# Kernel tuning notes

Measured on AMD Instinct MI355X. Metric: run time of the kernel, lower is better.

## Reference

```python
import jax, jax.numpy as jnp
import numpy as np

N_USER = 50000
N_ITEM = 100000
EMB = 64
NNZ = 1200000
BATCH = 4096
RATE = 0.1          # node_dropout[0]
N_LAYERS = 4        # len(layer_size); make_hop needs >=4 hops for 5 prefix means
N_NODES = N_USER + N_ITEM


def setup_inputs() -> dict:
    key = jax.random.key(0)
    ks = jax.random.split(key, 12)
    return {
        "user_emb": jax.random.normal(ks[0], (N_USER, EMB), dtype=jnp.float32) * 0.1,
        "item_emb": jax.random.normal(ks[1], (N_ITEM, EMB), dtype=jnp.float32) * 0.1,
        "adj_vals": jax.random.uniform(ks[2], (NNZ,), dtype=jnp.float32),
        "drop_u": jax.random.uniform(ks[3], (NNZ,), dtype=jnp.float32),
        "adj_rows": jax.random.randint(ks[4], (NNZ,), 0, N_NODES, dtype=jnp.int32),
        "adj_cols": jax.random.randint(ks[5], (NNZ,), 0, N_NODES, dtype=jnp.int32),
        "users": jax.random.randint(ks[6], (BATCH,), 0, N_USER, dtype=jnp.int32),
        "pos_items": jax.random.randint(ks[7], (BATCH,), 0, N_ITEM, dtype=jnp.int32),
        "neg_items": jax.random.randint(ks[8], (BATCH,), 0, N_ITEM, dtype=jnp.int32),
        "u_a": jax.random.randint(ks[9], (BATCH,), 0, 5, dtype=jnp.int32),
        "p_a": jax.random.randint(ks[10], (BATCH,), 0, 5, dtype=jnp.int32),
        "n_a": jax.random.randint(ks[11], (BATCH,), 0, 5, dtype=jnp.int32),
        "index": 0,
    }


def _make_hop(user_emb, item_emb, adj_vals, drop_u, adj_rows, adj_cols):
    # sparse dropout: floor(1 - rate + u) gives a 0/1 keep mask; rescale by 1/(1-rate).
    mask = jnp.floor((1.0 - RATE) + drop_u)
    vals = adj_vals * mask * (1.0 / (1.0 - RATE))
    ego = jnp.concatenate([user_emb, item_emb], axis=0)  # [N, d]
    all_embs = [ego]
    for _ in range(N_LAYERS):
        # SpMM: out[r] = sum_e vals[e] * ego[cols[e]] for rows[e] == r
        msgs = vals[:, None] * ego[adj_cols]             # [nnz, d]
        ego = jax.ops.segment_sum(msgs, adj_rows, num_segments=N_NODES)
        all_embs.append(ego)
    # prefix means over hops 0..i
    result = [all_embs[0]]
    running = all_embs[0]
    for i in range(1, 5):
        running = running + all_embs[i]
        result.append(running / float(i + 1))
    return jnp.stack(result)  # [5, N, d]


def reference(user_emb, item_emb, adj_vals, drop_u, adj_rows, adj_cols,
              users, pos_items, neg_items, u_a, p_a, n_a, index):
    embed = _make_hop(user_emb, item_emb, adj_vals, drop_u, adj_rows, adj_cols)
    n_user = user_emb.shape[0]
    if index == 0:
        u = embed[u_a, users]
        p = embed[p_a, pos_items + n_user]
        n = embed[n_a, neg_items + n_user]
    else:
        u = embed[u_a, users + n_user]
        p = embed[p_a, pos_items]
        n = embed[n_a, neg_items]
    return (u, p, n)
```

## Files before the change

### kernel.cpp

```cpp
#include <hip/hip_runtime.h>
#include <stdint.h>

#define N_USER_C  50000
#define N_ITEM_C  100000
#define N_NODES_C 150000
#define EMB_C     64
#define NNZ_C     1200000
#define BATCH_C   4096

#define BKT_SHIFT 9
#define BKT_ROWS  (1 << BKT_SHIFT)
#define NB        ((N_NODES_C + BKT_ROWS - 1) / BKT_ROWS)
#define CH        8192
#define NBLK      ((NNZ_C + CH - 1) / CH)
#define N2        (NB * NBLK)
#define COL_MASK  0x3FFFF

#define SPMM_B    37500
#define GB        3072
#define THB       2048

typedef _Float16 h16;
typedef _Float16 h16x4 __attribute__((ext_vector_type(4)));

__global__ __launch_bounds__(1024) void k_bin_count(const float* __restrict__ du,
                                                    const int* __restrict__ rows,
                                                    int* __restrict__ cnt2,
                                                    int* __restrict__ flagz) {
    __shared__ int bk[NB];
    int t = threadIdx.x, blk = blockIdx.x;
    for (int i = blk * 1024 + t; i < 2 * N_NODES_C; i += NBLK * 1024) flagz[i] = 0;
    for (int i = t; i < NB; i += 1024) bk[i] = 0;
    __syncthreads();
    int base = blk * CH;
    for (int i = 0; i < CH; i += 1024) {
        int e = base + i + t;
        if (e < NNZ_C && floorf(0.9f + du[e]) != 0.0f)
            atomicAdd(&bk[rows[e] >> BKT_SHIFT], 1);
    }
    __syncthreads();
    for (int i = t; i < NB; i += 1024) cnt2[i * NBLK + blk] = bk[i];
}

__global__ __launch_bounds__(512) void k_bbase(const int* __restrict__ cnt2,
                                               int* __restrict__ bbase,
                                               int* __restrict__ base2,
                                               int* __restrict__ row_start) {
    __shared__ int sh[512];
    int t = threadIdx.x;
    int s = 0;
    if (t < NB) {
        const int* p = cnt2 + t * NBLK;
        for (int i = 0; i < NBLK; ++i) s += p[i];
    }
    sh[t] = s;
    __syncthreads();
    for (int off = 1; off < 512; off <<= 1) {
        int v = (t >= off) ? sh[t - off] : 0;
        __syncthreads();
        sh[t] += v;
        __syncthreads();
    }
    if (t < NB) bbase[t] = sh[t] - s;
    if (t == 511) {
        base2[N2] = sh[511];
        row_start[N_NODES_C] = sh[511];
    }
}

__global__ __launch_bounds__(256) void k_bscan(const int* __restrict__ cnt2,
                                               const int* __restrict__ bbase,
                                               int* __restrict__ base2) {
    __shared__ int sh[256];
    int t = threadIdx.x, i = blockIdx.x;
    int v0 = (t < NBLK) ? cnt2[i * NBLK + t] : 0;
    sh[t] = v0;
    __syncthreads();
    for (int off = 1; off < 256; off <<= 1) {
        int v = (t >= off) ? sh[t - off] : 0;
        __syncthreads();
        sh[t] += v;
        __syncthreads();
    }
    if (t < NBLK) base2[i * NBLK + t] = bbase[i] + sh[t] - v0;
}

__global__ __launch_bounds__(1024) void k_bin_write(const float* __restrict__ av,
                                                    const float* __restrict__ du,
                                                    const int* __restrict__ rows,
                                                    const int* __restrict__ cols,
                                                    const int* __restrict__ base2,
                                                    int2* __restrict__ ev) {
    __shared__ int cur[NB];
    int t = threadIdx.x, blk = blockIdx.x;
    for (int i = t; i < NB; i += 1024) cur[i] = base2[i * NBLK + blk];
    __syncthreads();
    int base = blk * CH;
    for (int i = 0; i < CH; i += 1024) {
        int e = base + i + t;
        if (e < NNZ_C) {
            float m = floorf(0.9f + du[e]);
            if (m != 0.0f) {
                float v = av[e] * m * (float)(1.0 / 0.9);
                int r = rows[e];
                int pos = atomicAdd(&cur[r >> BKT_SHIFT], 1);
                int2 p;
                p.x = ((r & (BKT_ROWS - 1)) << 18) | cols[e];
                p.y = __float_as_int(v);
                ev[pos] = p;
            }
        }
    }
}

__global__ __launch_bounds__(256) void k_bucket_sort(const int2* __restrict__ ev,
                                                     const int* __restrict__ base2,
                                                     int2* __restrict__ ep,
                                                     int* __restrict__ row_start) {
    __shared__ int rowcnt[BKT_ROWS];
    __shared__ int cursor[BKT_ROWS];
    __shared__ int tsum[256];
    int t = threadIdx.x, k = blockIdx.x;
    int rowBase = k << BKT_SHIFT;
    int bstart = base2[k * NBLK];
    int bend   = base2[(k + 1) * NBLK];
    for (int i = t; i < BKT_ROWS; i += 256) rowcnt[i] = 0;
    __syncthreads();
    for (int e = bstart + t; e < bend; e += 256)
        atomicAdd(&rowcnt[((unsigned)ev[e].x) >> 18], 1);
    __syncthreads();
    int a = rowcnt[2 * t], b = rowcnt[2 * t + 1];
    tsum[t] = a + b;
    __syncthreads();
    for (int off = 1; off < 256; off <<= 1) {
        int v = (t >= off) ? tsum[t - off] : 0;
        __syncthreads();
        tsum[t] += v;
        __syncthreads();
    }
    int excl = tsum[t] - (a + b);
    cursor[2 * t]     = excl;
    cursor[2 * t + 1] = excl + a;
    int gr = rowBase + 2 * t;
    if (gr < N_NODES_C)     row_start[gr]     = bstart + excl;
    if (gr + 1 < N_NODES_C) row_start[gr + 1] = bstart + excl + a;
    __syncthreads();
    for (int e = bstart + t; e < bend; e += 256) {
        int2 p = ev[e];
        int rl = ((unsigned)p.x) >> 18;
        int slot = atomicAdd(&cursor[rl], 1);
        p.x &= COL_MASK;
        ep[bstart + slot] = p;
    }
}

__device__ __forceinline__ void batch_row_a(int wid, int idx0,
                                            const int* __restrict__ users,
                                            const int* __restrict__ pos,
                                            const int* __restrict__ neg,
                                            const int* __restrict__ ua,
                                            const int* __restrict__ pa,
                                            const int* __restrict__ na,
                                            int& row, int& a) {
    int s = wid >> 12;
    int j = wid & (BATCH_C - 1);
    if (s == 0)      { row = users[j] + (idx0 ? N_USER_C : 0); a = ua[j]; }
    else if (s == 1) { row = pos[j]   + (idx0 ? 0 : N_USER_C); a = pa[j]; }
    else             { row = neg[j]   + (idx0 ? 0 : N_USER_C); a = na[j]; }
}

__device__ __forceinline__ void spmm_row_body(int wid, int lane,
                                              const int* __restrict__ rs,
                                              const int2* __restrict__ ep,
                                              const h16x4* __restrict__ ego,
                                              h16x4* __restrict__ nxt,
                                              const int* __restrict__ flag) {
    if (wid >= N_NODES_C) return;
    if (flag && flag[wid] == 0) return;
    int start = rs[wid];
    int end   = rs[wid + 1];
    int eo = lane >> 4;
    int l  = lane & 15;
    float4 acc = make_float4(0.f, 0.f, 0.f, 0.f);
    #pragma unroll 2
    for (int it = start + eo; it < end; it += 4) {
        int2 p = ep[it];
        float v = __int_as_float(p.y);
        h16x4 g = ego[(int64_t)p.x * 16 + l];
        acc.x += v * (float)g[0]; acc.y += v * (float)g[1];
        acc.z += v * (float)g[2]; acc.w += v * (float)g[3];
    }
    acc.x += __shfl_xor(acc.x, 16); acc.y += __shfl_xor(acc.y, 16);
    acc.z += __shfl_xor(acc.z, 16); acc.w += __shfl_xor(acc.w, 16);
    acc.x += __shfl_xor(acc.x, 32); acc.y += __shfl_xor(acc.y, 32);
    acc.z += __shfl_xor(acc.z, 32); acc.w += __shfl_xor(acc.w, 32);
    if (lane < 16) {
        h16x4 h;
        h[0] = (h16)acc.x; h[1] = (h16)acc.y; h[2] = (h16)acc.z; h[3] = (h16)acc.w;
        nxt[(int64_t)wid * 16 + l] = h;
    }
}

__device__ __forceinline__ void gather_body(const h16* __restrict__ src,
                                            float* __restrict__ out, int t, int hop,
                                            int idx0,
                                            const int* __restrict__ users,
                                            const int* __restrict__ pos,
                                            const int* __restrict__ neg,
                                            const int* __restrict__ ua,
                                            const int* __restrict__ pa,
                                            const int* __restrict__ na) {
    int d = t & 63;
    int b = t >> 6;
    int row, a;
    batch_row_a(b, idx0, users, pos, neg, ua, pa, na, row, a);
    if (hop <= a)
        out[t] += (float)src[(int64_t)row * EMB_C + d] / (float)(a + 1);
}

__global__ __launch_bounds__(256) void k_prep(const float* __restrict__ ue,
                                              const float* __restrict__ ie,
                                              h16x4* __restrict__ dst,
                                              float* __restrict__ out,
                                              const int* __restrict__ users,
                                              const int* __restrict__ pos,
                                              const int* __restrict__ neg,
                                              const int* __restrict__ ua,
                                              const int* __restrict__ pa,
                                              const int* __restrict__ na,
                                              const int* __restrict__ indexp) {
    if (blockIdx.x < GB) {
        int t = blockIdx.x * 256 + threadIdx.x;
        int d = t & 63;
        int b = t >> 6;
        int row, a;
        batch_row_a(b, indexp[0], users, pos, neg, ua, pa, na, row, a);
        const float* sp = (row < N_USER_C) ? (ue + (int64_t)row * EMB_C)
                                           : (ie + (int64_t)(row - N_USER_C) * EMB_C);
        out[t] = sp[d] / (float)(a + 1);
    } else {
        const int totalU = N_USER_C * EMB_C / 4;
        const int total  = N_NODES_C * EMB_C / 4;
        const int stride = THB * 256;
        const float4* uev = (const float4*)ue;
        const float4* iev = (const float4*)ie;
        for (int i = (blockIdx.x - GB) * 256 + threadIdx.x; i < total; i += stride) {
            float4 v = (i < totalU) ? uev[i] : iev[i - totalU];
            h16x4 h;
            h[0] = (h16)v.x; h[1] = (h16)v.y; h[2] = (h16)v.z; h[3] = (h16)v.w;
            dst[i] = h;
        }
    }
}

__global__ __launch_bounds__(256) void k_spmm1f(const int* __restrict__ rs,
                                                const int2* __restrict__ ep,
                                                const h16x4* __restrict__ ego,
                                                h16x4* __restrict__ nxt,
                                                int* __restrict__ flag3,
                                                int* __restrict__ flag2,
                                                const int* __restrict__ users,
                                                const int* __restrict__ pos,
                                                const int* __restrict__ neg,
                                                const int* __restrict__ ua,
                                                const int* __restrict__ pa,
                                                const int* __restrict__ na,
                                                const int* __restrict__ indexp) {
    int lane = threadIdx.x & 63;
    if (blockIdx.x < SPMM_B) {
        int wid = (blockIdx.x * 256 + threadIdx.x) >> 6;
        spmm_row_body(wid, lane, rs, ep, ego, nxt, (const int*)nullptr);
    } else {
        int wid = ((blockIdx.x - SPMM_B) * 256 + threadIdx.x) >> 6;
        if (wid >= 3 * BATCH_C) return;
        int row, a;
        batch_row_a(wid, indexp[0], users, pos, neg, ua, pa, na, row, a);
        if (a < 2) return;
        if (lane == 0) {
            flag2[row] = 1;
            if (a >= 3) flag3[row] = 1;
        }
        if (a == 4) {
            int start = rs[row], end = rs[row + 1];
            for (int e = start + lane; e < end; e += 64)
                flag3[ep[e].x] = 1;
        }
    }
}

__global__ __launch_bounds__(256) void k_fg1(const int* __restrict__ rs,
                                             const int2* __restrict__ ep,
                                             const int* __restrict__ flag3,
                                             int* __restrict__ flag2,
                                             const h16* __restrict__ src,
                                             float* __restrict__ out,
                                             const int* __restrict__ users,
                                             const int* __restrict__ pos,
                                             const int* __restrict__ neg,
                                             const int* __restrict__ ua,
                                             const int* __restrict__ pa,
                                             const int* __restrict__ na,
                                             const int* __restrict__ indexp) {
    if (blockIdx.x < SPMM_B) {
        int wid  = (blockIdx.x * 256 + threadIdx.x) >> 6;
        int lane = threadIdx.x & 63;
        if (wid >= N_NODES_C || flag3[wid] == 0) return;
        int start = rs[wid], end = rs[wid + 1];
        for (int e = start + lane; e < end; e += 64)
            flag2[ep[e].x] = 1;
    } else {
        int t = (blockIdx.x - SPMM_B) * 256 + threadIdx.x;
        gather_body(src, out, t, 1, indexp[0], users, pos, neg, ua, pa, na);
    }
}

__global__ __launch_bounds__(256) void k_spmm2(const int* __restrict__ rs,
                                               const int2* __restrict__ ep,
                                               const h16x4* __restrict__ ego,
                                               h16x4* __restrict__ nxt,
                                               const int* __restrict__ flag) {
    int wid  = (blockIdx.x * 256 + threadIdx.x) >> 6;
    int lane = threadIdx.x & 63;
    spmm_row_body(wid, lane, rs, ep, ego, nxt, flag);
}

__global__ __launch_bounds__(256) void k_spmm3g2(const int* __restrict__ rs,
                                                 const int2* __restrict__ ep,
                                                 const h16x4* __restrict__ ego,
                                                 h16x4* __restrict__ nxt,
                                                 const int* __restrict__ flag3,
                                                 const h16* __restrict__ gsrc,
                                                 float* __restrict__ out,
                                                 const int* __restrict__ users,
                                                 const int* __restrict__ pos,
                                                 const int* __restrict__ neg,
                                                 const int* __restrict__ ua,
                                                 const int* __restrict__ pa,
                                                 const int* __restrict__ na,
                                                 const int* __restrict__ indexp) {
    if (blockIdx.x < SPMM_B) {
        int wid  = (blockIdx.x * 256 + threadIdx.x) >> 6;
        int lane = threadIdx.x & 63;
        spmm_row_body(wid, lane, rs, ep, ego, nxt, flag3);
    } else {
        int t = (blockIdx.x - SPMM_B) * 256 + threadIdx.x;
        gather_body(gsrc, out, t, 2, indexp[0], users, pos, neg, ua, pa, na);
    }
}

__global__ __launch_bounds__(256) void k_g3g4(const int* __restrict__ rs,
                                              const int2* __restrict__ ep,
                                              const h16x4* __restrict__ ego,
                                              float* __restrict__ out,
                                              const int* __restrict__ users,
                                              const int* __restrict__ pos,
                                              const int* __restrict__ neg,
                                              const int* __restrict__ ua,
                                              const int* __restrict__ pa,
                                              const int* __restrict__ na,
                                              const int* __restrict__ indexp) {
    int gid  = blockIdx.x * 256 + threadIdx.x;
    int wid  = gid >> 6;
    int lane = gid & 63;
    if (wid >= 3 * BATCH_C) return;
    int row, a;
    batch_row_a(wid, indexp[0], users, pos, neg, ua, pa, na, row, a);
    if (a < 3) return;
    float4 acc = make_float4(0.f, 0.f, 0.f, 0.f);
    if (a == 4) {
        int start = rs[row], end = rs[row + 1];
        int eo = lane >> 4;
        int l  = lane & 15;
        for (int it = start + eo; it < end; it += 4) {
            int2 p = ep[it];
            float v = __int_as_float(p.y);
            h16x4 g = ego[(int64_t)p.x * 16 + l];
            acc.x += v * (float)g[0]; acc.y += v * (float)g[1];
            acc.z += v * (float)g[2]; acc.w += v * (float)g[3];
        }
        acc.x += __shfl_xor(acc.x, 16); acc.y += __shfl_xor(acc.y, 16);
        acc.z += __shfl_xor(acc.z, 16); acc.w += __shfl_xor(acc.w, 16);
        acc.x += __shfl_xor(acc.x, 32); acc.y += __shfl_xor(acc.y, 32);
        acc.z += __shfl_xor(acc.z, 32); acc.w += __shfl_xor(acc.w, 32);
    }
    if (lane < 16) {
        h16x4 g = ego[(int64_t)row * 16 + lane];
        float inv = 1.0f / (float)(a + 1);
        float4* o = (float4*)out + (int64_t)wid * 16 + lane;
        float4 cv = *o;
        cv.x += ((float)g[0] + acc.x) * inv;
        cv.y += ((float)g[1] + acc.y) * inv;
        cv.z += ((float)g[2] + acc.z) * inv;
        cv.w += ((float)g[3] + acc.w) * inv;
        *o = cv;
    }
}

extern "C" void kernel_launch(void* const* d_in, const int* in_sizes, int n_in,
                              void* d_out, int out_size, void* d_ws, size_t ws_size,
                              hipStream_t stream) {
    const float* user_emb = (const float*)d_in[0];
    const float* item_emb = (const float*)d_in[1];
    const float* adj_vals = (const float*)d_in[2];
    const float* drop_u   = (const float*)d_in[3];
    const int*   adj_rows = (const int*)d_in[4];
    const int*   adj_cols = (const int*)d_in[5];
    const int*   users    = (const int*)d_in[6];
    const int*   pos_it   = (const int*)d_in[7];
    const int*   neg_it   = (const int*)d_in[8];
    const int*   u_a      = (const int*)d_in[9];
    const int*   p_a      = (const int*)d_in[10];
    const int*   n_a      = (const int*)d_in[11];
    const int*   indexp   = (const int*)d_in[12];
    float* out = (float*)d_out;

    const size_t egoElems = (size_t)N_NODES_C * EMB_C;
    h16*   egoH0     = (h16*)d_ws;
    h16*   bufA      = egoH0 + egoElems;
    h16*   bufB      = bufA + egoElems;
    int2*  ep        = (int2*)(bufB + egoElems);
    int2*  ev        = ep + NNZ_C;
    int*   row_start = (int*)(ev + NNZ_C);
    int*   cnt2      = row_start + N_NODES_C + 1;
    int*   base2     = cnt2 + N2 + 1;
    int*   bbase     = base2 + N2 + 1;
    int*   flags3    = bbase + NB + 1;
    int*   flags2    = flags3 + N_NODES_C;

    k_bin_count<<<NBLK, 1024, 0, stream>>>(drop_u, adj_rows, cnt2, flags3);
    k_bbase<<<1, 512, 0, stream>>>(cnt2, bbase, base2, row_start);
    k_bscan<<<NB, 256, 0, stream>>>(cnt2, bbase, base2);
    k_bin_write<<<NBLK, 1024, 0, stream>>>(adj_vals, drop_u, adj_rows, adj_cols,
                                           base2, ev);
    k_bucket_sort<<<NB, 256, 0, stream>>>(ev, base2, ep, row_start);

    k_prep<<<GB + THB, 256, 0, stream>>>(user_emb, item_emb, (h16x4*)egoH0, out,
                                         users, pos_it, neg_it, u_a, p_a, n_a, indexp);

    k_spmm1f<<<SPMM_B + GB, 256, 0, stream>>>(row_start, ep, (const h16x4*)egoH0,
                                              (h16x4*)bufA, flags3, flags2,
                                              users, pos_it, neg_it, u_a, p_a, n_a, indexp);
    k_fg1<<<SPMM_B + GB, 256, 0, stream>>>(row_start, ep, flags3, flags2,
                                           bufA, out,
                                           users, pos_it, neg_it, u_a, p_a, n_a, indexp);
    k_spmm2<<<SPMM_B, 256, 0, stream>>>(row_start, ep, (const h16x4*)bufA,
                                        (h16x4*)bufB, flags2);
    k_spmm3g2<<<SPMM_B + GB, 256, 0, stream>>>(row_start, ep, (const h16x4*)bufB,
                                               (h16x4*)bufA, flags3, bufB, out,
                                               users, pos_it, neg_it, u_a, p_a, n_a, indexp);
    k_g3g4<<<GB, 256, 0, stream>>>(row_start, ep, (const h16x4*)bufA, out,
                                   users, pos_it, neg_it, u_a, p_a, n_a, indexp);
}
```

Baseline: 194.1 us.

## Merge bucket-base scans into one kernel and move flag marking into prep

Replaces the single-block bucket-total scan plus per-bucket scan with one kernel in which each block recomputes its prefix by reducing all earlier counts. Separately, the batch-row flag-marking work moves from the first SpMM launch into the prep kernel as extra blocks, leaving a pure SpMM kernel. This removes a launch and a serial single-block step, at the cost of redundant reads of the count array (quadratic in bucket count) across blocks.

Measured after the change: 205.5 us. 1.06x slower.

```diff
diff --git a/kernel.cpp b/kernel.cpp
--- a/kernel.cpp
+++ b/kernel.cpp
@@ -19,6 +19,7 @@
 #define SPMM_B    37500
 #define GB        3072
 #define THB       2048
+#define FB        3072
 
 typedef _Float16 h16;
 typedef _Float16 h16x4 __attribute__((ext_vector_type(4)));
@@ -42,38 +43,23 @@
     for (int i = t; i < NB; i += 1024) cnt2[i * NBLK + blk] = bk[i];
 }
 
-__global__ __launch_bounds__(512) void k_bbase(const int* __restrict__ cnt2,
-                                               int* __restrict__ bbase,
-                                               int* __restrict__ base2,
-                                               int* __restrict__ row_start) {
-    __shared__ int sh[512];
-    int t = threadIdx.x;
-    int s = 0;
-    if (t < NB) {
-        const int* p = cnt2 + t * NBLK;
-        for (int i = 0; i < NBLK; ++i) s += p[i];
-    }
-    sh[t] = s;
-    __syncthreads();
-    for (int off = 1; off < 512; off <<= 1) {
-        int v = (t >= off) ? sh[t - off] : 0;
-        __syncthreads();
-        sh[t] += v;
-        __syncthreads();
-    }
-    if (t < NB) bbase[t] = sh[t] - s;
-    if (t == 511) {
-        base2[N2] = sh[511];
-        row_start[N_NODES_C] = sh[511];
-    }
-}
-
-__global__ __launch_bounds__(256) void k_bscan(const int* __restrict__ cnt2,
-                                               const int* __restrict__ bbase,
-                                               int* __restrict__ base2) {
+__global__ __launch_bounds__(256) void k_bscan2(const int* __restrict__ cnt2,
+                                                int* __restrict__ base2,
+                                                int* __restrict__ row_start) {
+    __shared__ int red[256];
     __shared__ int sh[256];
     int t = threadIdx.x, i = blockIdx.x;
-    int v0 = (t < NBLK) ? cnt2[i * NBLK + t] : 0;
+    int lim = i * NBLK;
+    int s = 0;
+    for (int idx = t; idx < lim; idx += 256) s += cnt2[idx];
+    red[t] = s;
+    __syncthreads();
+    for (int off = 128; off > 0; off >>= 1) {
+        if (t < off) red[t] += red[t + off];
+        __syncthreads();
+    }
+    int pre = red[0];
+    int v0 = (t < NBLK) ? cnt2[lim + t] : 0;
     sh[t] = v0;
     __syncthreads();
     for (int off = 1; off < 256; off <<= 1) {
@@ -82,7 +68,12 @@
         sh[t] += v;
         __syncthreads();
     }
-    if (t < NBLK) base2[i * NBLK + t] = bbase[i] + sh[t] - v0;
+    if (t < NBLK) base2[lim + t] = pre + sh[t] - v0;
+    if (i == NB - 1 && t == NBLK - 1) {
+        int total = pre + sh[t];
+        base2[N2] = total;
+        row_start[N_NODES_C] = total;
+    }
 }
 
 __global__ __launch_bounds__(1024) void k_bin_write(const float* __restrict__ av,
@@ -222,6 +213,10 @@
                                               const float* __restrict__ ie,
                                               h16x4* __restrict__ dst,
                                               float* __restrict__ out,
+                                              const int* __restrict__ rs,
+                                              const int2* __restrict__ ep,
+                                              int* __restrict__ flag3,
+                                              int* __restrict__ flag2,
                                               const int* __restrict__ users,
                                               const int* __restrict__ pos,
                                               const int* __restrict__ neg,
@@ -238,7 +233,7 @@
         const float* sp = (row < N_USER_C) ? (ue + (int64_t)row * EMB_C)
                                            : (ie + (int64_t)(row - N_USER_C) * EMB_C);
         out[t] = sp[d] / (float)(a + 1);
-    } else {
+    } else if (blockIdx.x < GB + THB) {
         const int totalU = N_USER_C * EMB_C / 4;
         const int total  = N_NODES_C * EMB_C / 4;
         const int stride = THB * 256;
@@ -250,28 +245,9 @@
             h[0] = (h16)v.x; h[1] = (h16)v.y; h[2] = (h16)v.z; h[3] = (h16)v.w;
             dst[i] = h;
         }
-    }
-}
-
-__global__ __launch_bounds__(256) void k_spmm1f(const int* __restrict__ rs,
-                                                const int2* __restrict__ ep,
-                                                const h16x4* __restrict__ ego,
-                                                h16x4* __restrict__ nxt,
-                                                int* __restrict__ flag3,
-                                                int* __restrict__ flag2,
-                                                const int* __restrict__ users,
-                                                const int* __restrict__ pos,
-                                                const int* __restrict__ neg,
-                                                const int* __restrict__ ua,
-                                                const int* __restrict__ pa,
-                                                const int* __restrict__ na,
-                                                const int* __restrict__ indexp) {
-    int lane = threadIdx.x & 63;
-    if (blockIdx.x < SPMM_B) {
-        int wid = (blockIdx.x * 256 + threadIdx.x) >> 6;
-        spmm_row_body(wid, lane, rs, ep, ego, nxt, (const int*)nullptr);
     } else {
-        int wid = ((blockIdx.x - SPMM_B) * 256 + threadIdx.x) >> 6;
+        int wid  = ((blockIdx.x - GB - THB) * 256 + threadIdx.x) >> 6;
+        int lane = threadIdx.x & 63;
         if (wid >= 3 * BATCH_C) return;
         int row, a;
         batch_row_a(wid, indexp[0], users, pos, neg, ua, pa, na, row, a);
@@ -286,6 +262,15 @@
                 flag3[ep[e].x] = 1;
         }
     }
+}
+
+__global__ __launch_bounds__(256) void k_spmm1(const int* __restrict__ rs,
+                                               const int2* __restrict__ ep,
+                                               const h16x4* __restrict__ ego,
+                                               h16x4* __restrict__ nxt) {
+    int wid  = (blockIdx.x * 256 + threadIdx.x) >> 6;
+    int lane = threadIdx.x & 63;
+    spmm_row_body(wid, lane, rs, ep, ego, nxt, (const int*)nullptr);
 }
 
 __global__ __launch_bounds__(256) void k_fg1(const int* __restrict__ rs,
@@ -423,23 +408,21 @@
     int*   row_start = (int*)(ev + NNZ_C);
     int*   cnt2      = row_start + N_NODES_C + 1;
     int*   base2     = cnt2 + N2 + 1;
-    int*   bbase     = base2 + N2 + 1;
-    int*   flags3    = bbase + NB + 1;
+    int*   flags3    = base2 + N2 + 1;
     int*   flags2    = flags3 + N_NODES_C;
 
     k_bin_count<<<NBLK, 1024, 0, stream>>>(drop_u, adj_rows, cnt2, flags3);
-    k_bbase<<<1, 512, 0, stream>>>(cnt2, bbase, base2, row_start);
-    k_bscan<<<NB, 256, 0, stream>>>(cnt2, bbase, base2);
+    k_bscan2<<<NB, 256, 0, stream>>>(cnt2, base2, row_start);
     k_bin_write<<<NBLK, 1024, 0, stream>>>(adj_vals, drop_u, adj_rows, adj_cols,
                                            base2, ev);
     k_bucket_sort<<<NB, 256, 0, stream>>>(ev, base2, ep, row_start);
 
-    k_prep<<<GB + THB, 256, 0, stream>>>(user_emb, item_emb, (h16x4*)egoH0, out,
-                                         users, pos_it, neg_it, u_a, p_a, n_a, indexp);
-
-    k_spmm1f<<<SPMM_B + GB, 256, 0, stream>>>(row_start, ep, (const h16x4*)egoH0,
-                                              (h16x4*)bufA, flags3, flags2,
+    k_prep<<<GB + THB + FB, 256, 0, stream>>>(user_emb, item_emb, (h16x4*)egoH0, out,
+                                              row_start, ep, flags3, flags2,
                                               users, pos_it, neg_it, u_a, p_a, n_a, indexp);
+
+    k_spmm1<<<SPMM_B, 256, 0, stream>>>(row_start, ep, (const h16x4*)egoH0,
+                                        (h16x4*)bufA);
     k_fg1<<<SPMM_B + GB, 256, 0, stream>>>(row_start, ep, flags3, flags2,
                                            bufA, out,
                                            users, pos_it, neg_it, u_a, p_a, n_a, indexp);
```

## Reschedule flag marking and hop-1 gather to drop one kernel launch

Applied to the files above, without the earlier changes.

Moves the batch-based flag3/flag2 seeding into extra blocks of k_prep. The flag3-to-flag2 propagation now runs as extra blocks of the first SpMM kernel, and the hop-1 gather is merged into the second SpMM kernel. This removes one launch and its grid-wide barrier. The cost is larger fused grids, and correctness now depends on the new ordering: flag3 must be complete before the propagation runs, and flag2 must be complete before spmm2.

Measured after the change: 192.1 us. Within noise of the previous version (-1.1%).

```diff
diff --git a/kernel.cpp b/kernel.cpp
--- a/kernel.cpp
+++ b/kernel.cpp
@@ -19,6 +19,7 @@
 #define SPMM_B    37500
 #define GB        3072
 #define THB       2048
+#define FB        3072
 
 typedef _Float16 h16;
 typedef _Float16 h16x4 __attribute__((ext_vector_type(4)));
@@ -222,6 +223,10 @@
                                               const float* __restrict__ ie,
                                               h16x4* __restrict__ dst,
                                               float* __restrict__ out,
+                                              const int* __restrict__ rs,
+                                              const int2* __restrict__ ep,
+                                              int* __restrict__ flag3,
+                                              int* __restrict__ flag2,
                                               const int* __restrict__ users,
                                               const int* __restrict__ pos,
                                               const int* __restrict__ neg,
@@ -238,7 +243,7 @@
         const float* sp = (row < N_USER_C) ? (ue + (int64_t)row * EMB_C)
                                            : (ie + (int64_t)(row - N_USER_C) * EMB_C);
         out[t] = sp[d] / (float)(a + 1);
-    } else {
+    } else if (blockIdx.x < GB + THB) {
         const int totalU = N_USER_C * EMB_C / 4;
         const int total  = N_NODES_C * EMB_C / 4;
         const int stride = THB * 256;
@@ -250,28 +255,9 @@
             h[0] = (h16)v.x; h[1] = (h16)v.y; h[2] = (h16)v.z; h[3] = (h16)v.w;
             dst[i] = h;
         }
-    }
-}
-
-__global__ __launch_bounds__(256) void k_spmm1f(const int* __restrict__ rs,
-                                                const int2* __restrict__ ep,
-                                                const h16x4* __restrict__ ego,
-                                                h16x4* __restrict__ nxt,
-                                                int* __restrict__ flag3,
-                                                int* __restrict__ flag2,
-                                                const int* __restrict__ users,
-                                                const int* __restrict__ pos,
-                                                const int* __restrict__ neg,
-                                                const int* __restrict__ ua,
-                                                const int* __restrict__ pa,
-                                                const int* __restrict__ na,
-                                                const int* __restrict__ indexp) {
-    int lane = threadIdx.x & 63;
-    if (blockIdx.x < SPMM_B) {
-        int wid = (blockIdx.x * 256 + threadIdx.x) >> 6;
-        spmm_row_body(wid, lane, rs, ep, ego, nxt, (const int*)nullptr);
     } else {
-        int wid = ((blockIdx.x - SPMM_B) * 256 + threadIdx.x) >> 6;
+        int wid  = ((blockIdx.x - GB - THB) * 256 + threadIdx.x) >> 6;
+        int lane = threadIdx.x & 63;
         if (wid >= 3 * BATCH_C) return;
         int row, a;
         batch_row_a(wid, indexp[0], users, pos, neg, ua, pa, na, row, a);
@@ -288,40 +274,47 @@
     }
 }
 
-__global__ __launch_bounds__(256) void k_fg1(const int* __restrict__ rs,
-                                             const int2* __restrict__ ep,
-                                             const int* __restrict__ flag3,
-                                             int* __restrict__ flag2,
-                                             const h16* __restrict__ src,
-                                             float* __restrict__ out,
-                                             const int* __restrict__ users,
-                                             const int* __restrict__ pos,
-                                             const int* __restrict__ neg,
-                                             const int* __restrict__ ua,
-                                             const int* __restrict__ pa,
-                                             const int* __restrict__ na,
-                                             const int* __restrict__ indexp) {
+__global__ __launch_bounds__(256) void k_spmm1f(const int* __restrict__ rs,
+                                                const int2* __restrict__ ep,
+                                                const h16x4* __restrict__ ego,
+                                                h16x4* __restrict__ nxt,
+                                                const int* __restrict__ flag3,
+                                                int* __restrict__ flag2) {
+    int lane = threadIdx.x & 63;
     if (blockIdx.x < SPMM_B) {
-        int wid  = (blockIdx.x * 256 + threadIdx.x) >> 6;
-        int lane = threadIdx.x & 63;
+        int wid = (blockIdx.x * 256 + threadIdx.x) >> 6;
+        spmm_row_body(wid, lane, rs, ep, ego, nxt, (const int*)nullptr);
+    } else {
+        int wid = ((blockIdx.x - SPMM_B) * 256 + threadIdx.x) >> 6;
         if (wid >= N_NODES_C || flag3[wid] == 0) return;
         int start = rs[wid], end = rs[wid + 1];
         for (int e = start + lane; e < end; e += 64)
             flag2[ep[e].x] = 1;
+    }
+}
+
+__global__ __launch_bounds__(256) void k_spmm2g1(const int* __restrict__ rs,
+                                                 const int2* __restrict__ ep,
+                                                 const h16x4* __restrict__ ego,
+                                                 h16x4* __restrict__ nxt,
+                                                 const int* __restrict__ flag2,
+                                                 const h16* __restrict__ gsrc,
+                                                 float* __restrict__ out,
+                                                 const int* __restrict__ users,
+                                                 const int* __restrict__ pos,
+                                                 const int* __restrict__ neg,
+                                                 const int* __restrict__ ua,
+                                                 const int* __restrict__ pa,
+                                                 const int* __restrict__ na,
+                                                 const int* __restrict__ indexp) {
+    if (blockIdx.x < SPMM_B) {
+        int wid  = (blockIdx.x * 256 + threadIdx.x) >> 6;
+        int lane = threadIdx.x & 63;
+        spmm_row_body(wid, lane, rs, ep, ego, nxt, flag2);
     } else {
         int t = (blockIdx.x - SPMM_B) * 256 + threadIdx.x;
-        gather_body(src, out, t, 1, indexp[0], users, pos, neg, ua, pa, na);
-    }
-}
-
-__global__ __launch_bounds__(256) void k_spmm2(const int* __restrict__ rs,
-                                               const int2* __restrict__ ep,
-                                               const h16x4* __restrict__ ego,
-                                               h16x4* __restrict__ nxt,
-                                               const int* __restrict__ flag) {
-    int wid  = (blockIdx.x * 256 + threadIdx.x) >> 6;
-    int lane = threadIdx.x & 63;
-    spmm_row_body(wid, lane, rs, ep, ego, nxt, flag);
+        gather_body(gsrc, out, t, 1, indexp[0], users, pos, neg, ua, pa, na);
+    }
 }
 
 __global__ __launch_bounds__(256) void k_spmm3g2(const int* __restrict__ rs,
@@ -434,17 +427,15 @@
                                            base2, ev);
     k_bucket_sort<<<NB, 256, 0, stream>>>(ev, base2, ep, row_start);
 
-    k_prep<<<GB + THB, 256, 0, stream>>>(user_emb, item_emb, (h16x4*)egoH0, out,
-                                         users, pos_it, neg_it, u_a, p_a, n_a, indexp);
-
-    k_spmm1f<<<SPMM_B + GB, 256, 0, stream>>>(row_start, ep, (const h16x4*)egoH0,
-                                              (h16x4*)bufA, flags3, flags2,
+    k_prep<<<GB + THB + FB, 256, 0, stream>>>(user_emb, item_emb, (h16x4*)egoH0, out,
+                                              row_start, ep, flags3, flags2,
                                               users, pos_it, neg_it, u_a, p_a, n_a, indexp);
-    k_fg1<<<SPMM_B + GB, 256, 0, stream>>>(row_start, ep, flags3, flags2,
-                                           bufA, out,
-                                           users, pos_it, neg_it, u_a, p_a, n_a, indexp);
-    k_spmm2<<<SPMM_B, 256, 0, stream>>>(row_start, ep, (const h16x4*)bufA,
-                                        (h16x4*)bufB, flags2);
+
+    k_spmm1f<<<SPMM_B + SPMM_B, 256, 0, stream>>>(row_start, ep, (const h16x4*)egoH0,
+                                                  (h16x4*)bufA, flags3, flags2);
+    k_spmm2g1<<<SPMM_B + GB, 256, 0, stream>>>(row_start, ep, (const h16x4*)bufA,
+                                               (h16x4*)bufB, flags2, bufA, out,
+                                               users, pos_it, neg_it, u_a, p_a, n_a, indexp);
     k_spmm3g2<<<SPMM_B + GB, 256, 0, stream>>>(row_start, ep, (const h16x4*)bufB,
                                                (h16x4*)bufA, flags3, bufB, out,
                                                users, pos_it, neg_it, u_a, p_a, n_a, indexp);
```
